# Kernel tuning notes

Measured on AMD Instinct MI355X. Metric: run time of the kernel, lower is better.

## Reference

```python
import jax, jax.numpy as jnp
import numpy as np

LN_EPS = 1e-5  # torch.nn.LayerNorm default eps


def setup_inputs() -> dict:
    key = jax.random.key(0)
    k1, k2 = jax.random.split(key)
    x = jax.random.normal(k1, (16384, 2048), dtype=jnp.float32)
    # torch Linear weight layout: [out_features, in_features]
    W = jax.random.normal(k2, (2048, 2048), dtype=jnp.float32) * (1.0 / np.sqrt(2048))
    return {"x": x, "W": W}


def reference(x, W):
    # LayerNorm over last dim, elementwise_affine=False
    mean = jnp.mean(x, axis=-1, keepdims=True)
    var = jnp.mean(jnp.square(x - mean), axis=-1, keepdims=True)
    xn = (x - mean) * jax.lax.rsqrt(var + LN_EPS)
    # Linear (no bias): y = xn @ W.T, then sigmoid
    y = jnp.einsum("td,od->to", xn, W)
    return jax.nn.sigmoid(y)
```

## Files before the change

### kernel.cpp

```cpp
#include <hip/hip_runtime.h>
#include <hip/hip_bf16.h>
#include <stdint.h>


typedef __attribute__((ext_vector_type(4))) float f32x4;
typedef __attribute__((ext_vector_type(8))) __bf16 b16x8;

__device__ __forceinline__ void async16(void* lds_p, const void* g) {
  __builtin_amdgcn_global_load_lds(
      (const __attribute__((address_space(1))) void*)g,
      (__attribute__((address_space(3))) void*)lds_p, 16, 0, 0);
}

__device__ __forceinline__ unsigned short f2bf(float f) {
  uint32_t u = __float_as_uint(f);
  u += 0x7FFFu + ((u >> 16) & 1u);
  return (unsigned short)(u >> 16);
}

__global__ __launch_bounds__(256) void ln_wconv_kernel(
    const float* __restrict__ x, unsigned short* __restrict__ xn,
    const float* __restrict__ W, unsigned short* __restrict__ Wb) {
  const int t = threadIdx.x;
  if (blockIdx.x >= 16384) {
    const size_t i = (size_t)(blockIdx.x - 16384) * 256 + t;
    float4 v = ((const float4*)W)[i];
    ushort4 o;
    o.x = f2bf(v.x); o.y = f2bf(v.y); o.z = f2bf(v.z); o.w = f2bf(v.w);
    ((ushort4*)Wb)[i] = o;
    return;
  }
  const int row = blockIdx.x;
  const float4* xr = (const float4*)(x + (size_t)row * 2048);
  float4 a = xr[t];
  float4 b = xr[t + 256];
  float s = a.x + a.y + a.z + a.w + b.x + b.y + b.z + b.w;
  float q = a.x * a.x + a.y * a.y + a.z * a.z + a.w * a.w +
            b.x * b.x + b.y * b.y + b.z * b.z + b.w * b.w;
#pragma unroll
  for (int off = 32; off > 0; off >>= 1) {
    s += __shfl_down(s, off);
    q += __shfl_down(q, off);
  }
  __shared__ float red[8];
  const int w = t >> 6;
  if ((t & 63) == 0) { red[w] = s; red[4 + w] = q; }
  __syncthreads();
  s = red[0] + red[1] + red[2] + red[3];
  q = red[4] + red[5] + red[6] + red[7];
  const float mean = s * (1.0f / 2048.0f);
  const float var = fmaxf(q * (1.0f / 2048.0f) - mean * mean, 0.0f);
  const float scl = rsqrtf(var + 1e-5f);
  ushort4 o0, o1;
  o0.x = f2bf((a.x - mean) * scl);
  o0.y = f2bf((a.y - mean) * scl);
  o0.z = f2bf((a.z - mean) * scl);
  o0.w = f2bf((a.w - mean) * scl);
  o1.x = f2bf((b.x - mean) * scl);
  o1.y = f2bf((b.y - mean) * scl);
  o1.z = f2bf((b.z - mean) * scl);
  o1.w = f2bf((b.w - mean) * scl);
  ushort4* orow = (ushort4*)(xn + (size_t)row * 2048);
  orow[t] = o0;
  orow[t + 256] = o1;
}


#define STG(BOFF, KT)                                                  \
  do {                                                                 \
    const char* sA_ = pA + (size_t)(KT) * 128;                         \
    const char* sB_ = pB + (size_t)(KT) * 128;                         \
    char* d_ = lds + (BOFF) + tid * 16;                                \
    async16(d_, sA_);                                                  \
    async16(d_ + 16384, sA_ + (size_t)128 * 4096);                     \
    async16(d_ + 32768, sB_);                                          \
    async16(d_ + 49152, sB_ + (size_t)128 * 4096);                     \
  } while (0)

#define LDA_S(BOFF, S)                                                 \
  do {                                                                 \
    _Pragma("unroll") for (int i_ = 0; i_ < 4; ++i_) {                 \
      const char* p_ = lds + (BOFF) + abase + i_ * 2048;               \
      aF[i_][S] = *(const b16x8*)(p_ + ((S) ? cs1 : cs0));             \
    }                                                                  \
  } while (0)

#define LDB_S(BOFF, S)                                                 \
  do {                                                                 \
    _Pragma("unroll") for (int j_ = 0; j_ < 4; ++j_) {                 \
      const char* p_ = lds + (BOFF) + bbase + j_ * 2048;               \
      bF[j_][S] = *(const b16x8*)(p_ + ((S) ? cs1 : cs0));             \
    }                                                                  \
  } while (0)

#define MFMA_IJ(ILO, IHI, S)                                           \
  do {                                                                 \
    __builtin_amdgcn_s_setprio(1);                                     \
    _Pragma("unroll") for (int i_ = (ILO); i_ < (IHI); ++i_) {         \
      _Pragma("unroll") for (int j_ = 0; j_ < 4; ++j_) {               \
        acc[i_][j_] = __builtin_amdgcn_mfma_f32_16x16x32_bf16(         \
            aF[i_][S], bF[j_][S], acc[i_][j_], 0, 0, 0);               \
      }                                                                \
    }                                                                  \
    __builtin_amdgcn_s_setprio(0);                                     \
  } while (0)

#define BARR                                                           \
  do {                                                                 \
    __builtin_amdgcn_s_barrier();                                      \
    asm volatile("" ::: "memory");                                     \
  } while (0)

#define LGKM0                                                          \
  do {                                                                 \
    asm volatile("s_waitcnt lgkmcnt(0)" ::: "memory");                 \
    __builtin_amdgcn_sched_barrier(0);                                 \
  } while (0)

#define SB0 __builtin_amdgcn_sched_barrier(0)
#define VMC(n) asm volatile("s_waitcnt vmcnt(" #n ")" ::: "memory")

__global__ __launch_bounds__(1024, 4) void gemm16w(
    const unsigned short* __restrict__ A, const unsigned short* __restrict__ B,
    float* __restrict__ C) {
  __shared__ __align__(16) char lds[131072];

  const int bid0 = blockIdx.x;
  const int bid = (bid0 & 7) * 64 + (bid0 >> 3);
  const int bm = bid >> 3;
  const int bn = bid & 7;

  const int tid = threadIdx.x;
  const int w = tid >> 6, l = tid & 63;
  const int wr = w >> 2, wc = w & 3;
  const int fr = l & 15, fg = l >> 4;

  const int arow = tid >> 3;
  const int swz = ((tid & 7) << 4) ^ ((arow & 7) << 4);
  const char* pA = (const char*)A + (size_t)(bm * 256 + arow) * 4096 + swz;
  const char* pB = (const char*)B + (size_t)(bn * 256 + arow) * 4096 + swz;

  const int cswz = (fg << 4) ^ ((fr & 7) << 4);
  const int cs0 = cswz, cs1 = cswz ^ 64;
  const int abase = (wr * 64 + fr) * 128;
  const int bbase = 32768 + (wc * 64 + fr) * 128;

  f32x4 acc[4][4] = {};
  b16x8 aF[4][2], bF[4][2];

  STG(0, 0);
  VMC(0);
  BARR;

#pragma unroll 1
  for (int t = 0; t < 32; ++t) {
    const int cur = (t & 1) * 65536;
    const int nxt = 65536 - cur;

    if (t < 31) { STG(nxt, t + 1); VMC(4); } else { VMC(0); }
    SB0;
    LDA_S(cur, 0); LDB_S(cur, 0);
    LGKM0;
    MFMA_IJ(0, 2, 0);
    SB0; LDA_S(cur, 1); LDB_S(cur, 1); SB0;
    MFMA_IJ(2, 4, 0);
    LGKM0;
    MFMA_IJ(0, 4, 1);
    BARR;
  }

  float* gC = C + (size_t)(bm * 256 + wr * 64) * 2048 + bn * 256 + wc * 64;
#pragma unroll
  for (int i = 0; i < 4; ++i) {
#pragma unroll
    for (int j = 0; j < 4; ++j) {
#pragma unroll
      for (int r = 0; r < 4; ++r) {
        const int row = i * 16 + fg * 4 + r;
        const int col = j * 16 + fr;
        const float y = acc[i][j][r];
        gC[(size_t)row * 2048 + col] =
            __builtin_amdgcn_rcpf(1.0f + __expf(-y));
      }
    }
  }
}

extern "C" void kernel_launch(void* const* d_in, const int* in_sizes, int n_in,
                              void* d_out, int out_size, void* d_ws, size_t ws_size,
                              hipStream_t stream) {
  const float* x = (const float*)d_in[0];
  const float* W = (const float*)d_in[1];
  float* out = (float*)d_out;

  unsigned short* xnb = (unsigned short*)d_ws;
  unsigned short* Wb =
      (unsigned short*)((char*)d_ws + (size_t)16384 * 2048 * 2);

  ln_wconv_kernel<<<16384 + 4096, 256, 0, stream>>>(x, xnb, W, Wb);
  gemm16w<<<512, 1024, 0, stream>>>(xnb, Wb, out);
}
```

Baseline: 178.9 us.

## Load B fragments directly from global into registers, stage only A in LDS

New measurement: 227.3 us. 1.27x slower.

```diff
diff --git a/kernel.cpp b/kernel.cpp
--- a/kernel.cpp
+++ b/kernel.cpp
@@ -66,43 +66,39 @@
 }
 
 
-#define STG(BOFF, KT)                                                  \
+#define STG_A(BOFF, h, kt)                                             \
   do {                                                                 \
-    const char* sA_ = pA + (size_t)(KT) * 128;                         \
-    const char* sB_ = pB + (size_t)(KT) * 128;                         \
-    char* d_ = lds + (BOFF) + tid * 16;                                \
-    async16(d_, sA_);                                                  \
-    async16(d_ + 16384, sA_ + (size_t)128 * 4096);                     \
-    async16(d_ + 32768, sB_);                                          \
-    async16(d_ + 49152, sB_ + (size_t)128 * 4096);                     \
+    const char* s_ = pA + (size_t)((h) * 128) * 4096 + (kt) * 128;     \
+    char* d_ = lds + (BOFF) + (h) * 16384 + tid * 16;                  \
+    async16(d_, s_);                                                   \
+    async16(d_ + 8192, s_ + 64 * 4096);                                \
   } while (0)
 
-#define LDA_S(BOFF, S)                                                 \
+#define LDA8(BOFF, DST, S)                                             \
   do {                                                                 \
-    _Pragma("unroll") for (int i_ = 0; i_ < 4; ++i_) {                 \
-      const char* p_ = lds + (BOFF) + abase + i_ * 2048;               \
-      aF[i_][S] = *(const b16x8*)(p_ + ((S) ? cs1 : cs0));             \
+    _Pragma("unroll") for (int m_ = 0; m_ < 8; ++m_) {                 \
+      const char* p_ = lds + (BOFF) + (m_ >> 2) * 16384 + abase +      \
+                       (m_ & 3) * 2048;                                \
+      DST[m_] = *(const b16x8*)(p_ + ((S) ? cs1 : cs0));               \
     }                                                                  \
   } while (0)
 
-#define LDB_S(BOFF, S)                                                 \
+#define LDG_B_S(KT, S)                                                 \
   do {                                                                 \
-    _Pragma("unroll") for (int j_ = 0; j_ < 4; ++j_) {                 \
-      const char* p_ = lds + (BOFF) + bbase + j_ * 2048;               \
-      bF[j_][S] = *(const b16x8*)(p_ + ((S) ? cs1 : cs0));             \
-    }                                                                  \
+    bF[0][S] = *(const b16x8*)(pBv + (size_t)(KT) * 128 + (S) * 64);   \
+    bF[1][S] = *(const b16x8*)(pBv + 65536 + (size_t)(KT) * 128 + (S) * 64); \
+    bF[2][S] = *(const b16x8*)(pBv + 524288 + (size_t)(KT) * 128 + (S) * 64); \
+    bF[3][S] = *(const b16x8*)(pBv + 589824 + (size_t)(KT) * 128 + (S) * 64); \
   } while (0)
 
-#define MFMA_IJ(ILO, IHI, S)                                           \
+#define MFMA_MN(AF, MLO, MHI, S)                                       \
   do {                                                                 \
-    __builtin_amdgcn_s_setprio(1);                                     \
-    _Pragma("unroll") for (int i_ = (ILO); i_ < (IHI); ++i_) {         \
-      _Pragma("unroll") for (int j_ = 0; j_ < 4; ++j_) {               \
-        acc[i_][j_] = __builtin_amdgcn_mfma_f32_16x16x32_bf16(         \
-            aF[i_][S], bF[j_][S], acc[i_][j_], 0, 0, 0);               \
+    _Pragma("unroll") for (int m_ = (MLO); m_ < (MHI); ++m_) {         \
+      _Pragma("unroll") for (int n_ = 0; n_ < 4; ++n_) {               \
+        acc[m_][n_] = __builtin_amdgcn_mfma_f32_16x16x32_bf16(         \
+            AF[m_], bF[n_][S], acc[m_][n_], 0, 0, 0);                  \
       }                                                                \
     }                                                                  \
-    __builtin_amdgcn_s_setprio(0);                                     \
   } while (0)
 
 #define BARR                                                           \
@@ -111,24 +107,17 @@
     asm volatile("" ::: "memory");                                     \
   } while (0)
 
-#define LGKM0                                                          \
-  do {                                                                 \
-    asm volatile("s_waitcnt lgkmcnt(0)" ::: "memory");                 \
-    __builtin_amdgcn_sched_barrier(0);                                 \
-  } while (0)
-
 #define SB0 __builtin_amdgcn_sched_barrier(0)
 #define VMC(n) asm volatile("s_waitcnt vmcnt(" #n ")" ::: "memory")
 
-__global__ __launch_bounds__(1024, 4) void gemm16w(
+__global__ __launch_bounds__(512, 2) void gemm_bd(
     const unsigned short* __restrict__ A, const unsigned short* __restrict__ B,
     float* __restrict__ C) {
-  __shared__ __align__(16) char lds[131072];
+  __shared__ __align__(16) char lds[65536];
 
   const int bid0 = blockIdx.x;
-  const int bid = (bid0 & 7) * 64 + (bid0 >> 3);
-  const int bm = bid >> 3;
-  const int bn = bid & 7;
+  const int bn = bid0 & 7;
+  const int bm = bid0 >> 3;
 
   const int tid = threadIdx.x;
   const int w = tid >> 6, l = tid & 63;
@@ -138,47 +127,52 @@
   const int arow = tid >> 3;
   const int swz = ((tid & 7) << 4) ^ ((arow & 7) << 4);
   const char* pA = (const char*)A + (size_t)(bm * 256 + arow) * 4096 + swz;
-  const char* pB = (const char*)B + (size_t)(bn * 256 + arow) * 4096 + swz;
+
+  const char* pBv =
+      (const char*)B + (size_t)(bn * 256 + wc * 32 + fr) * 4096 + fg * 16;
 
   const int cswz = (fg << 4) ^ ((fr & 7) << 4);
   const int cs0 = cswz, cs1 = cswz ^ 64;
   const int abase = (wr * 64 + fr) * 128;
-  const int bbase = 32768 + (wc * 64 + fr) * 128;
 
-  f32x4 acc[4][4] = {};
-  b16x8 aF[4][2], bF[4][2];
+  f32x4 acc[8][4] = {};
+  b16x8 aFa[8], aFb[8], bF[4][2];
 
-  STG(0, 0);
-  VMC(0);
+  STG_A(0, 0, 0); STG_A(0, 1, 0);
+  LDG_B_S(0, 0); LDG_B_S(0, 1);
+  VMC(8);
   BARR;
 
 #pragma unroll 1
   for (int t = 0; t < 32; ++t) {
-    const int cur = (t & 1) * 65536;
-    const int nxt = 65536 - cur;
+    const int cur = (t & 1) << 15;
+    const int nxt = 32768 - cur;
+    const bool s2 = (t < 31);
 
-    if (t < 31) { STG(nxt, t + 1); VMC(4); } else { VMC(0); }
-    SB0;
-    LDA_S(cur, 0); LDB_S(cur, 0);
-    LGKM0;
-    MFMA_IJ(0, 2, 0);
-    SB0; LDA_S(cur, 1); LDB_S(cur, 1); SB0;
-    MFMA_IJ(2, 4, 0);
-    LGKM0;
-    MFMA_IJ(0, 4, 1);
-    BARR;
+    LDA8(cur, aFa, 0);
+    if (s2) { STG_A(nxt, 0, t + 1); STG_A(nxt, 1, t + 1); }
+    MFMA_MN(aFa, 0, 4, 0);
+    SB0; LDA8(cur, aFb, 1); SB0;
+    MFMA_MN(aFa, 4, 8, 0);
+    if (s2) { SB0; LDG_B_S(t + 1, 0); SB0; }
+    MFMA_MN(aFb, 0, 8, 1);
+    if (s2) { SB0; LDG_B_S(t + 1, 1); SB0; }
+    if (s2) {
+      VMC(8);
+      BARR;
+    }
   }
 
-  float* gC = C + (size_t)(bm * 256 + wr * 64) * 2048 + bn * 256 + wc * 64;
+  float* gC = C + (size_t)(bm * 256) * 2048 + bn * 256;
 #pragma unroll
-  for (int i = 0; i < 4; ++i) {
+  for (int m = 0; m < 8; ++m) {
 #pragma unroll
-    for (int j = 0; j < 4; ++j) {
+    for (int n = 0; n < 4; ++n) {
+      const int col = (n >> 1) * 128 + wc * 32 + (n & 1) * 16 + fr;
 #pragma unroll
       for (int r = 0; r < 4; ++r) {
-        const int row = i * 16 + fg * 4 + r;
-        const int col = j * 16 + fr;
-        const float y = acc[i][j][r];
+        const int row = (m >> 2) * 128 + wr * 64 + (m & 3) * 16 + fg * 4 + r;
+        const float y = acc[m][n][r];
         gC[(size_t)row * 2048 + col] =
             __builtin_amdgcn_rcpf(1.0f + __expf(-y));
       }
@@ -198,5 +192,5 @@
       (unsigned short*)((char*)d_ws + (size_t)16384 * 2048 * 2);
 
   ln_wconv_kernel<<<16384 + 4096, 256, 0, stream>>>(x, xnb, W, Wb);
-  gemm16w<<<512, 1024, 0, stream>>>(xnb, Wb, out);
+  gemm_bd<<<512, 512, 0, stream>>>(xnb, Wb, out);
 }
```
